# Kernel optimization log

Hardware: AMD Instinct MI355X
Metric: run time of the kernel (lower is better)

Reference implementation:

```python
import jax, jax.numpy as jnp
import numpy as np

B, N, F_IN, F_OUT = 8, 2048, 128, 64
ALPHA = 0.2  # LeakyReLU negative slope
NEG_BIG = -9e15


def setup_inputs() -> dict:
    key = jax.random.key(0)
    k1, k2, k3, k4 = jax.random.split(key, 4)
    x = jax.random.normal(k1, (B, N, F_IN), dtype=jnp.float32)
    adj = jax.random.randint(k2, (B, N, N), 0, 2, dtype=jnp.int32)
    # xavier-uniform-ish init scale for faithfulness (gain=1.414)
    w_lim = 1.414 * np.sqrt(6.0 / (F_IN + F_OUT))
    a_lim = 1.414 * np.sqrt(6.0 / (2 * F_OUT + 1))
    weight = jax.random.uniform(k3, (F_IN, F_OUT), minval=-w_lim, maxval=w_lim, dtype=jnp.float32)
    weight2 = jax.random.uniform(k4, (2 * F_OUT, 1), minval=-a_lim, maxval=a_lim, dtype=jnp.float32)
    return {"x": x, "adj": adj, "weight": weight, "weight2": weight2}


def reference(x, adj, weight, weight2):
    # Linear projection: [B, N, F_out]
    wh = jnp.einsum("bnf,fo->bno", x, weight)
    # Additive GAT decomposition of concat-score:
    # e_ij = leakyrelu(a1 . Wh_i + a2 . Wh_j)  == original concat @ weight2
    a1 = weight2[:F_OUT, 0]   # [F_out]
    a2 = weight2[F_OUT:, 0]   # [F_out]
    s1 = wh @ a1              # [B, N]
    s2 = wh @ a2              # [B, N]
    e = s1[:, :, None] + s2[:, None, :]          # [B, N, N]
    e = jnp.where(e > 0, e, ALPHA * e)            # LeakyReLU
    e = jnp.where(adj > 0, e, NEG_BIG)            # mask non-edges
    attention = jax.nn.softmax(e, axis=2)         # [B, N, N]
    # dropout is identity in eval mode (training=False)
    out = jnp.einsum("bij,bjo->bio", attention, wh)  # [B, N, F_out]
    return jax.nn.elu(out)
```

## Files before the change

kernel.cpp:

```cpp
#include <hip/hip_runtime.h>
#include <cstdint>
#include <cstddef>

#define B_    8
#define N_    2048
#define FIN   128
#define FOUT  64
#define ALPHA 0.2f
#define LOG2E 1.4426950408889634f

typedef __attribute__((ext_vector_type(8))) _Float16 half8;
typedef __attribute__((ext_vector_type(4))) _Float16 half4;
typedef __attribute__((ext_vector_type(4))) float float4v;

__global__ __launch_bounds__(256) void k0_convW(
    const float* __restrict__ W, _Float16* __restrict__ WtG)
{
    int o = blockIdx.x * 256 + threadIdx.x;
    int f = o >> 7, k = o & 127;
    float v = W[k * FOUT + f];
    _Float16 hi = (_Float16)v;
    _Float16 lo = (_Float16)(v - (float)hi);
    WtG[o] = hi;
    WtG[FOUT * FIN + o] = lo;
}

__global__ __launch_bounds__(256, 2) void k1_wh(
    const float* __restrict__ x, const _Float16* __restrict__ WtG,
    const float* __restrict__ w2, _Float16* __restrict__ whT,
    float* __restrict__ s1, float* __restrict__ s2)
{
    __shared__ __attribute__((aligned(16))) _Float16 xth[32][136];
    __shared__ __attribute__((aligned(16))) _Float16 xtl[32][136];
    __shared__ float s1p[4][32];
    __shared__ float s2p[4][32];

    int t = threadIdx.x, lane = t & 63, w = t >> 6;
    int b = blockIdx.x >> 6;
    int r0 = (blockIdx.x & 63) << 5;
    const float* xb = x + ((size_t)b * N_ + r0) * FIN;

    #pragma unroll
    for (int j = 0; j < 4; ++j) {
        int idx = t + j * 256;
        int row = idx >> 5;
        int k0 = (idx & 31) * 4;
        float4 v = ((const float4*)xb)[idx];
        float vv[4] = {v.x, v.y, v.z, v.w};
        half4 h, l;
        #pragma unroll
        for (int e = 0; e < 4; ++e) {
            _Float16 hi = (_Float16)vv[e];
            h[e] = hi;
            l[e] = (_Float16)(vv[e] - (float)hi);
        }
        *(half4*)&xth[row][k0] = h;
        *(half4*)&xtl[row][k0] = l;
    }
    __syncthreads();

    int l15 = lane & 15, quad = lane >> 4;
    int f0 = w * 16;

    half8 bh[4], bl[4];
    const _Float16* wgh = WtG + (f0 + l15) * FIN + quad * 8;
    #pragma unroll
    for (int c = 0; c < 4; ++c) {
        bh[c] = *(const half8*)(wgh + c * 32);
        bl[c] = *(const half8*)(wgh + FOUT * FIN + c * 32);
    }
    float a1f = w2[f0 + l15], a2f = w2[FOUT + f0 + l15];

    #pragma unroll
    for (int rt = 0; rt < 2; ++rt) {
        float4v acc = {0.f, 0.f, 0.f, 0.f};
        #pragma unroll
        for (int c = 0; c < 4; ++c) {
            half8 ah = *(const half8*)&xth[rt * 16 + l15][c * 32 + quad * 8];
            half8 al = *(const half8*)&xtl[rt * 16 + l15][c * 32 + quad * 8];
            acc = __builtin_amdgcn_mfma_f32_16x16x32_f16(ah, bh[c], acc, 0, 0, 0);
            acc = __builtin_amdgcn_mfma_f32_16x16x32_f16(ah, bl[c], acc, 0, 0, 0);
            acc = __builtin_amdgcn_mfma_f32_16x16x32_f16(al, bh[c], acc, 0, 0, 0);
        }
        half4 hv;
        #pragma unroll
        for (int reg = 0; reg < 4; ++reg) hv[reg] = (_Float16)acc[reg];
        *(half4*)(whT + ((size_t)b * FOUT + f0 + l15) * N_ + r0 + rt * 16 + quad * 4) = hv;

        #pragma unroll
        for (int reg = 0; reg < 4; ++reg) {
            float v1 = acc[reg] * a1f;
            float v2 = acc[reg] * a2f;
            #pragma unroll
            for (int m = 1; m <= 8; m <<= 1) {
                v1 += __shfl_xor(v1, m);
                v2 += __shfl_xor(v2, m);
            }
            if (l15 == 0) {
                s1p[w][rt * 16 + quad * 4 + reg] = v1;
                s2p[w][rt * 16 + quad * 4 + reg] = v2;
            }
        }
    }
    __syncthreads();
    if (t < 32) {
        float v = s1p[0][t] + s1p[1][t] + s1p[2][t] + s1p[3][t];
        s1[(size_t)b * N_ + r0 + t] = v;
    } else if (t < 64) {
        int r = t - 32;
        float v = s2p[0][r] + s2p[1][r] + s2p[2][r] + s2p[3][r];
        s2[(size_t)b * N_ + r0 + r] = v;
    }
}

__global__ __launch_bounds__(256, 4) void k2_attn(
    const int* __restrict__ adj, const _Float16* __restrict__ whT,
    const float* __restrict__ s1, const float* __restrict__ s2,
    float* __restrict__ out)
{
    __shared__ __attribute__((aligned(16))) int adjS[2][16][256];
    __shared__ __attribute__((aligned(16))) _Float16 pT[2][16][264];
    __shared__ float lL[16];
    __shared__ float smaxL[4];

    int t = threadIdx.x, lane = t & 63, w = t >> 6;
    int b = blockIdx.x >> 7;
    int i0 = (blockIdx.x & 127) << 4;

    const float4* s2v = (const float4*)(s2 + (size_t)b * N_);
    float4 ua_ = s2v[t], ub_ = s2v[t + 256];
    float vm = fmaxf(fmaxf(fmaxf(ua_.x, ua_.y), fmaxf(ua_.z, ua_.w)),
                     fmaxf(fmaxf(ub_.x, ub_.y), fmaxf(ub_.z, ub_.w)));
    #pragma unroll
    for (int m = 32; m >= 1; m >>= 1) vm = fmaxf(vm, __shfl_xor(vm, m));
    if (lane == 0) smaxL[w] = vm;
    __syncthreads();
    float s2max = fmaxf(fmaxf(smaxL[0], smaxL[1]), fmaxf(smaxL[2], smaxL[3]));

    int l15 = lane & 15, quad = lane >> 4;
    int f0 = w * 16;

    float c1[4], c2[4], lacc[4];
    #pragma unroll
    for (int rr = 0; rr < 4; ++rr) {
        float sv = s1[(size_t)b * N_ + i0 + w * 4 + rr];
        float mm = sv + s2max;
        float mh = fmaxf(mm, ALPHA * mm);
        c1[rr] = (sv - mh) * LOG2E;
        c2[rr] = (ALPHA * sv - mh) * LOG2E;
        lacc[rr] = 0.f;
    }

    const int* adjL = adj + ((size_t)b * N_ + i0 + w * 4) * N_ + lane * 4;
    const float* s2L = s2 + (size_t)b * N_ + lane * 4;
    float4 Sb[2];

#define STAGE(cn, bf) do {                                                   \
        _Pragma("unroll")                                                    \
        for (int rr = 0; rr < 4; ++rr) {                                     \
            const int* src_ = adjL + (size_t)rr * N_ + (cn) * 256;           \
            __builtin_amdgcn_global_load_lds(                                \
                (const __attribute__((address_space(1))) void*)src_,         \
                (__attribute__((address_space(3))) void*)&adjS[bf][w * 4 + rr][0], \
                16, 0, 0);                                                   \
        }                                                                    \
        Sb[bf] = *(const float4*)(s2L + (cn) * 256);                         \
    } while (0)

    STAGE(0, 0);

    float4v acc = {0.f, 0.f, 0.f, 0.f};
    const _Float16* wB = whT + ((size_t)b * FOUT + f0 + l15) * N_ + quad * 8;

    #pragma unroll
    for (int c = 0; c < 8; ++c) {
        half8 bfr[8];
        const _Float16* wp = wB + c * 256;
        #pragma unroll
        for (int kk = 0; kk < 8; ++kk) bfr[kk] = *(const half8*)(wp + kk * 32);

        if (c < 7) {
            STAGE(c + 1, (c + 1) & 1);
            asm volatile("s_waitcnt vmcnt(13)" ::: "memory");
        } else {
            asm volatile("s_waitcnt vmcnt(8)" ::: "memory");
        }
        __builtin_amdgcn_sched_barrier(0);

        {
            float4 sv = Sb[c & 1];
            float u[4]  = {sv.x * LOG2E, sv.y * LOG2E, sv.z * LOG2E, sv.w * LOG2E};
            float ua[4] = {u[0] * ALPHA, u[1] * ALPHA, u[2] * ALPHA, u[3] * ALPHA};
            #pragma unroll
            for (int rr = 0; rr < 4; ++rr) {
                int r = w * 4 + rr;
                int4 av = *(const int4*)&adjS[c & 1][r][lane * 4];
                int aa[4] = {av.x, av.y, av.z, av.w};
                half4 pf;
                float ls = 0.f;
                #pragma unroll
                for (int e = 0; e < 4; ++e) {
                    float tt = fmaxf(c1[rr] + u[e], c2[rr] + ua[e]);
#if __has_builtin(__builtin_amdgcn_exp2f)
                    float p = __builtin_amdgcn_exp2f(tt);
#else
                    float p = exp2f(tt);
#endif
                    p = (aa[e] > 0) ? p : 0.f;
                    ls += p;
                    pf[e] = (_Float16)p;
                }
                lacc[rr] += ls;
                *(half4*)&pT[c & 1][r][lane * 4] = pf;
            }
        }

        if (c == 7) {
            #pragma unroll
            for (int rr = 0; rr < 4; ++rr) {
                float v = lacc[rr];
                #pragma unroll
                for (int m = 32; m >= 1; m >>= 1) v += __shfl_xor(v, m);
                if (lane == 0) lL[w * 4 + rr] = v;
            }
        }

        __syncthreads();

        #pragma unroll
        for (int kk = 0; kk < 8; ++kk) {
            half8 af = *(const half8*)&pT[c & 1][l15][kk * 32 + quad * 8];
            acc = __builtin_amdgcn_mfma_f32_16x16x32_f16(af, bfr[kk], acc, 0, 0, 0);
        }
    }
#undef STAGE

    #pragma unroll
    for (int reg = 0; reg < 4; ++reg) {
        int row = quad * 4 + reg;
        float val = acc[reg] / lL[row];
        val = (val > 0.f) ? val : (__expf(val) - 1.f);
        out[((size_t)b * N_ + i0 + row) * FOUT + f0 + l15] = val;
    }
}

extern "C" void kernel_launch(void* const* d_in, const int* in_sizes, int n_in,
                              void* d_out, int out_size, void* d_ws, size_t ws_size,
                              hipStream_t stream) {
    const float* x   = (const float*)d_in[0];
    const int*   adj = (const int*)d_in[1];
    const float* W   = (const float*)d_in[2];
    const float* w2  = (const float*)d_in[3];
    float* out = (float*)d_out;

    _Float16* whT = (_Float16*)d_ws;
    float* s1 = (float*)((char*)d_ws + (size_t)B_ * FOUT * N_ * 2);
    float* s2 = s1 + (size_t)B_ * N_;
    _Float16* WtG = (_Float16*)(s2 + (size_t)B_ * N_);

    k0_convW<<<32, 256, 0, stream>>>(W, WtG);
    k1_wh<<<(B_ * N_) / 32, 256, 0, stream>>>(x, WtG, w2, whT, s1, s2);
    k2_attn<<<(B_ * N_) / 16, 256, 0, stream>>>(adj, whT, s1, s2, out);
}
```

Measured before the change: 214.0 us.

## Pre-pack adjacency into bitmasks and read bits in attention kernel

Adds a kernel that turns the int32 adjacency matrix into 64-bit ballot bitmasks, one bit per edge. The attention kernel then loads a few mask words per row chunk instead of streaming int32 adjacency through LDS, and the async global-to-LDS double-buffering is removed. The aim is to shrink memory traffic and LDS use in the attention kernel. The cost is that the full adjacency is still read once, now in a separate pass, plus an extra launch, and the attention loads are no longer prefetched ahead of compute.

```diff
diff --git a/kernel.cpp b/kernel.cpp
--- a/kernel.cpp
+++ b/kernel.cpp
@@ -23,6 +23,21 @@
     _Float16 lo = (_Float16)(v - (float)hi);
     WtG[o] = hi;
     WtG[FOUT * FIN + o] = lo;
+}
+
+__global__ __launch_bounds__(256) void kp_pack(
+    const int* __restrict__ adj, unsigned long long* __restrict__ maskp)
+{
+    int t = threadIdx.x, lane = t & 63, w = t >> 6;
+    size_t row = (size_t)blockIdx.x * 4 + w;
+    const int* rp = adj + row * N_ + lane;
+    unsigned long long* orow = maskp + row * 32;
+    #pragma unroll
+    for (int it = 0; it < 32; ++it) {
+        int a = rp[it * 64];
+        unsigned long long m = __ballot(a > 0);
+        if (lane == 0) orow[it] = m;
+    }
 }
 
 __global__ __launch_bounds__(256, 2) void k1_wh(
@@ -114,11 +129,10 @@
 }
 
 __global__ __launch_bounds__(256, 4) void k2_attn(
-    const int* __restrict__ adj, const _Float16* __restrict__ whT,
+    const unsigned long long* __restrict__ maskp, const _Float16* __restrict__ whT,
     const float* __restrict__ s1, const float* __restrict__ s2,
     float* __restrict__ out)
 {
-    __shared__ __attribute__((aligned(16))) int adjS[2][16][256];
     __shared__ __attribute__((aligned(16))) _Float16 pT[2][16][264];
     __shared__ float lL[16];
     __shared__ float smaxL[4];
@@ -139,6 +153,7 @@
 
     int l15 = lane & 15, quad = lane >> 4;
     int f0 = w * 16;
+    int sh4 = l15 * 4;
 
     float c1[4], c2[4], lacc[4];
     #pragma unroll
@@ -151,68 +166,48 @@
         lacc[rr] = 0.f;
     }
 
-    const int* adjL = adj + ((size_t)b * N_ + i0 + w * 4) * N_ + lane * 4;
+    const unsigned long long* mB =
+        maskp + ((size_t)b * N_ + i0 + w * 4) * 32 + (lane >> 4);
     const float* s2L = s2 + (size_t)b * N_ + lane * 4;
-    float4 Sb[2];
-
-#define STAGE(cn, bf) do {                                                   \
-        _Pragma("unroll")                                                    \
-        for (int rr = 0; rr < 4; ++rr) {                                     \
-            const int* src_ = adjL + (size_t)rr * N_ + (cn) * 256;           \
-            __builtin_amdgcn_global_load_lds(                                \
-                (const __attribute__((address_space(1))) void*)src_,         \
-                (__attribute__((address_space(3))) void*)&adjS[bf][w * 4 + rr][0], \
-                16, 0, 0);                                                   \
-        }                                                                    \
-        Sb[bf] = *(const float4*)(s2L + (cn) * 256);                         \
-    } while (0)
-
-    STAGE(0, 0);
 
     float4v acc = {0.f, 0.f, 0.f, 0.f};
     const _Float16* wB = whT + ((size_t)b * FOUT + f0 + l15) * N_ + quad * 8;
 
     #pragma unroll
     for (int c = 0; c < 8; ++c) {
+        unsigned mbits[4];
+        #pragma unroll
+        for (int rr = 0; rr < 4; ++rr) {
+            unsigned long long mw = mB[(size_t)rr * 32 + c * 4];
+            mbits[rr] = (unsigned)(mw >> sh4) & 0xFu;
+        }
+        float4 sv = *(const float4*)(s2L + c * 256);
         half8 bfr[8];
         const _Float16* wp = wB + c * 256;
         #pragma unroll
         for (int kk = 0; kk < 8; ++kk) bfr[kk] = *(const half8*)(wp + kk * 32);
 
-        if (c < 7) {
-            STAGE(c + 1, (c + 1) & 1);
-            asm volatile("s_waitcnt vmcnt(13)" ::: "memory");
-        } else {
-            asm volatile("s_waitcnt vmcnt(8)" ::: "memory");
-        }
-        __builtin_amdgcn_sched_barrier(0);
-
-        {
-            float4 sv = Sb[c & 1];
-            float u[4]  = {sv.x * LOG2E, sv.y * LOG2E, sv.z * LOG2E, sv.w * LOG2E};
-            float ua[4] = {u[0] * ALPHA, u[1] * ALPHA, u[2] * ALPHA, u[3] * ALPHA};
+        float u[4]  = {sv.x * LOG2E, sv.y * LOG2E, sv.z * LOG2E, sv.w * LOG2E};
+        float ua[4] = {u[0] * ALPHA, u[1] * ALPHA, u[2] * ALPHA, u[3] * ALPHA};
+        #pragma unroll
+        for (int rr = 0; rr < 4; ++rr) {
+            int r = w * 4 + rr;
+            half4 pf;
+            float ls = 0.f;
             #pragma unroll
-            for (int rr = 0; rr < 4; ++rr) {
-                int r = w * 4 + rr;
-                int4 av = *(const int4*)&adjS[c & 1][r][lane * 4];
-                int aa[4] = {av.x, av.y, av.z, av.w};
-                half4 pf;
-                float ls = 0.f;
-                #pragma unroll
-                for (int e = 0; e < 4; ++e) {
-                    float tt = fmaxf(c1[rr] + u[e], c2[rr] + ua[e]);
+            for (int e = 0; e < 4; ++e) {
+                float tt = fmaxf(c1[rr] + u[e], c2[rr] + ua[e]);
 #if __has_builtin(__builtin_amdgcn_exp2f)
-                    float p = __builtin_amdgcn_exp2f(tt);
+                float p = __builtin_amdgcn_exp2f(tt);
 #else
-                    float p = exp2f(tt);
+                float p = exp2f(tt);
 #endif
-                    p = (aa[e] > 0) ? p : 0.f;
-                    ls += p;
-                    pf[e] = (_Float16)p;
-                }
-                lacc[rr] += ls;
-                *(half4*)&pT[c & 1][r][lane * 4] = pf;
-            }
+                p = (mbits[rr] & (1u << e)) ? p : 0.f;
+                ls += p;
+                pf[e] = (_Float16)p;
+            }
+            lacc[rr] += ls;
+            *(half4*)&pT[c & 1][r][lane * 4] = pf;
         }
 
         if (c == 7) {
@@ -233,7 +228,6 @@
             acc = __builtin_amdgcn_mfma_f32_16x16x32_f16(af, bfr[kk], acc, 0, 0, 0);
         }
     }
-#undef STAGE
 
     #pragma unroll
     for (int reg = 0; reg < 4; ++reg) {
@@ -253,12 +247,16 @@
     const float* w2  = (const float*)d_in[3];
     float* out = (float*)d_out;
 
-    _Float16* whT = (_Float16*)d_ws;
-    float* s1 = (float*)((char*)d_ws + (size_t)B_ * FOUT * N_ * 2);
-    float* s2 = s1 + (size_t)B_ * N_;
-    _Float16* WtG = (_Float16*)(s2 + (size_t)B_ * N_);
+    char* ws = (char*)d_ws;
+    _Float16* whT = (_Float16*)ws;
+    float* s1  = (float*)(ws + 2097152);
+    float* s2  = (float*)(ws + 2097152 + 65536);
+    _Float16* WtG = (_Float16*)(ws + 2097152 + 131072);
+    unsigned long long* maskp =
+        (unsigned long long*)(ws + 2097152 + 131072 + 32768);
 
     k0_convW<<<32, 256, 0, stream>>>(W, WtG);
+    kp_pack<<<(B_ * N_) / 4, 256, 0, stream>>>(adj, maskp);
     k1_wh<<<(B_ * N_) / 32, 256, 0, stream>>>(x, WtG, w2, whT, s1, s2);
-    k2_attn<<<(B_ * N_) / 16, 256, 0, stream>>>(adj, whT, s1, s2, out);
-}
+    k2_attn<<<(B_ * N_) / 16, 256, 0, stream>>>(maskp, whT, s1, s2, out);
+}
```

Result: slower. 268.3 us (+25.4%).

## Fuse weight conversion into projection kernel and double attention block rows

Applied to the files above, without the earlier changes.

Drops the separate weight-conversion kernel. The projection kernel now reads fp32 weights directly and does the hi/lo fp16 split in registers, saving one launch at the cost of strided global reads per block. The attention kernel moves to 512-thread blocks covering 32 rows as two 16-row tiles, which halves the block count and shares the s2 max reduction across more rows. The B-fragment whT loads are not shared between tiles, and launch bounds (512,1) with double the shared memory may lower occupancy.

```diff
diff --git a/kernel.cpp b/kernel.cpp
--- a/kernel.cpp
+++ b/kernel.cpp
@@ -13,22 +13,10 @@
 typedef __attribute__((ext_vector_type(4))) _Float16 half4;
 typedef __attribute__((ext_vector_type(4))) float float4v;
 
-__global__ __launch_bounds__(256) void k0_convW(
-    const float* __restrict__ W, _Float16* __restrict__ WtG)
-{
-    int o = blockIdx.x * 256 + threadIdx.x;
-    int f = o >> 7, k = o & 127;
-    float v = W[k * FOUT + f];
-    _Float16 hi = (_Float16)v;
-    _Float16 lo = (_Float16)(v - (float)hi);
-    WtG[o] = hi;
-    WtG[FOUT * FIN + o] = lo;
-}
-
 __global__ __launch_bounds__(256, 2) void k1_wh(
-    const float* __restrict__ x, const _Float16* __restrict__ WtG,
-    const float* __restrict__ w2, _Float16* __restrict__ whT,
-    float* __restrict__ s1, float* __restrict__ s2)
+    const float* __restrict__ x, const float* __restrict__ W,
+    const float* __restrict__ w2,
+    _Float16* __restrict__ whT, float* __restrict__ s1, float* __restrict__ s2)
 {
     __shared__ __attribute__((aligned(16))) _Float16 xth[32][136];
     __shared__ __attribute__((aligned(16))) _Float16 xtl[32][136];
@@ -63,11 +51,16 @@
     int f0 = w * 16;
 
     half8 bh[4], bl[4];
-    const _Float16* wgh = WtG + (f0 + l15) * FIN + quad * 8;
+    const float* wcol = W + (f0 + l15);
     #pragma unroll
     for (int c = 0; c < 4; ++c) {
-        bh[c] = *(const half8*)(wgh + c * 32);
-        bl[c] = *(const half8*)(wgh + FOUT * FIN + c * 32);
+        #pragma unroll
+        for (int e = 0; e < 8; ++e) {
+            float v = wcol[(size_t)(c * 32 + quad * 8 + e) * FOUT];
+            _Float16 hi = (_Float16)v;
+            bh[c][e] = hi;
+            bl[c][e] = (_Float16)(v - (float)hi);
+        }
     }
     float a1f = w2[f0 + l15], a2f = w2[FOUT + f0 + l15];
 
@@ -113,37 +106,41 @@
     }
 }
 
-__global__ __launch_bounds__(256, 4) void k2_attn(
+__global__ __launch_bounds__(512, 1) void k2_attn(
     const int* __restrict__ adj, const _Float16* __restrict__ whT,
     const float* __restrict__ s1, const float* __restrict__ s2,
     float* __restrict__ out)
 {
-    __shared__ __attribute__((aligned(16))) int adjS[2][16][256];
-    __shared__ __attribute__((aligned(16))) _Float16 pT[2][16][264];
-    __shared__ float lL[16];
-    __shared__ float smaxL[4];
+    __shared__ __attribute__((aligned(16))) int adjS[2][32][256];
+    __shared__ __attribute__((aligned(16))) _Float16 pT[2][2][16][264];
+    __shared__ float lL[2][16];
+    __shared__ float smaxL[8];
 
     int t = threadIdx.x, lane = t & 63, w = t >> 6;
-    int b = blockIdx.x >> 7;
-    int i0 = (blockIdx.x & 127) << 4;
+    int b = blockIdx.x >> 6;
+    int i0 = (blockIdx.x & 63) << 5;
+    int tile = w >> 2;
+    int wq = w & 3;
+    int rbase = i0 + tile * 16;
 
     const float4* s2v = (const float4*)(s2 + (size_t)b * N_);
-    float4 ua_ = s2v[t], ub_ = s2v[t + 256];
-    float vm = fmaxf(fmaxf(fmaxf(ua_.x, ua_.y), fmaxf(ua_.z, ua_.w)),
-                     fmaxf(fmaxf(ub_.x, ub_.y), fmaxf(ub_.z, ub_.w)));
+    float4 uv = s2v[t];
+    float vm = fmaxf(fmaxf(uv.x, uv.y), fmaxf(uv.z, uv.w));
     #pragma unroll
     for (int m = 32; m >= 1; m >>= 1) vm = fmaxf(vm, __shfl_xor(vm, m));
     if (lane == 0) smaxL[w] = vm;
     __syncthreads();
-    float s2max = fmaxf(fmaxf(smaxL[0], smaxL[1]), fmaxf(smaxL[2], smaxL[3]));
+    float s2max = smaxL[0];
+    #pragma unroll
+    for (int i = 1; i < 8; ++i) s2max = fmaxf(s2max, smaxL[i]);
 
     int l15 = lane & 15, quad = lane >> 4;
-    int f0 = w * 16;
+    int f0 = wq * 16;
 
     float c1[4], c2[4], lacc[4];
     #pragma unroll
     for (int rr = 0; rr < 4; ++rr) {
-        float sv = s1[(size_t)b * N_ + i0 + w * 4 + rr];
+        float sv = s1[(size_t)b * N_ + rbase + wq * 4 + rr];
         float mm = sv + s2max;
         float mh = fmaxf(mm, ALPHA * mm);
         c1[rr] = (sv - mh) * LOG2E;
@@ -151,7 +148,7 @@
         lacc[rr] = 0.f;
     }
 
-    const int* adjL = adj + ((size_t)b * N_ + i0 + w * 4) * N_ + lane * 4;
+    const int* adjL = adj + ((size_t)b * N_ + rbase + wq * 4) * N_ + lane * 4;
     const float* s2L = s2 + (size_t)b * N_ + lane * 4;
     float4 Sb[2];
 
@@ -161,7 +158,8 @@
             const int* src_ = adjL + (size_t)rr * N_ + (cn) * 256;           \
             __builtin_amdgcn_global_load_lds(                                \
                 (const __attribute__((address_space(1))) void*)src_,         \
-                (__attribute__((address_space(3))) void*)&adjS[bf][w * 4 + rr][0], \
+                (__attribute__((address_space(3))) void*)                    \
+                    &adjS[bf][tile * 16 + wq * 4 + rr][0],                   \
                 16, 0, 0);                                                   \
         }                                                                    \
         Sb[bf] = *(const float4*)(s2L + (cn) * 256);                         \
@@ -193,7 +191,7 @@
             float ua[4] = {u[0] * ALPHA, u[1] * ALPHA, u[2] * ALPHA, u[3] * ALPHA};
             #pragma unroll
             for (int rr = 0; rr < 4; ++rr) {
-                int r = w * 4 + rr;
+                int r = tile * 16 + wq * 4 + rr;
                 int4 av = *(const int4*)&adjS[c & 1][r][lane * 4];
                 int aa[4] = {av.x, av.y, av.z, av.w};
                 half4 pf;
@@ -211,7 +209,7 @@
                     pf[e] = (_Float16)p;
                 }
                 lacc[rr] += ls;
-                *(half4*)&pT[c & 1][r][lane * 4] = pf;
+                *(half4*)&pT[c & 1][tile][wq * 4 + rr][lane * 4] = pf;
             }
         }
 
@@ -221,7 +219,7 @@
                 float v = lacc[rr];
                 #pragma unroll
                 for (int m = 32; m >= 1; m >>= 1) v += __shfl_xor(v, m);
-                if (lane == 0) lL[w * 4 + rr] = v;
+                if (lane == 0) lL[tile][wq * 4 + rr] = v;
             }
         }
 
@@ -229,7 +227,7 @@
 
         #pragma unroll
         for (int kk = 0; kk < 8; ++kk) {
-            half8 af = *(const half8*)&pT[c & 1][l15][kk * 32 + quad * 8];
+            half8 af = *(const half8*)&pT[c & 1][tile][l15][kk * 32 + quad * 8];
             acc = __builtin_amdgcn_mfma_f32_16x16x32_f16(af, bfr[kk], acc, 0, 0, 0);
         }
     }
@@ -238,9 +236,9 @@
     #pragma unroll
     for (int reg = 0; reg < 4; ++reg) {
         int row = quad * 4 + reg;
-        float val = acc[reg] / lL[row];
+        float val = acc[reg] / lL[tile][row];
         val = (val > 0.f) ? val : (__expf(val) - 1.f);
-        out[((size_t)b * N_ + i0 + row) * FOUT + f0 + l15] = val;
+        out[((size_t)b * N_ + rbase + row) * FOUT + f0 + l15] = val;
     }
 }
 
@@ -253,12 +251,11 @@
     const float* w2  = (const float*)d_in[3];
     float* out = (float*)d_out;
 
-    _Float16* whT = (_Float16*)d_ws;
-    float* s1 = (float*)((char*)d_ws + (size_t)B_ * FOUT * N_ * 2);
-    float* s2 = s1 + (size_t)B_ * N_;
-    _Float16* WtG = (_Float16*)(s2 + (size_t)B_ * N_);
-
-    k0_convW<<<32, 256, 0, stream>>>(W, WtG);
-    k1_wh<<<(B_ * N_) / 32, 256, 0, stream>>>(x, WtG, w2, whT, s1, s2);
-    k2_attn<<<(B_ * N_) / 16, 256, 0, stream>>>(adj, whT, s1, s2, out);
+    char* ws = (char*)d_ws;
+    _Float16* whT = (_Float16*)ws;
+    float* s1  = (float*)(ws + 2097152);
+    float* s2  = (float*)(ws + 2097152 + 65536);
+
+    k1_wh<<<(B_ * N_) / 32, 256, 0, stream>>>(x, W, w2, whT, s1, s2);
+    k2_attn<<<(B_ * N_) / 32, 512, 0, stream>>>(adj, whT, s1, s2, out);
 }
```

Result: slower. 219.0 us (+2.3%).
